# Kernel tuning notes

Hardware: AMD Instinct MI355X
Metric: run time of the kernel (lower is better)

The kernel has to match this reference:

```python
import jax, jax.numpy as jnp
import numpy as np
from math import sqrt

HEADS = 16
DIM_HEAD = 64
BETA = 1.0 / sqrt(DIM_HEAD)


def setup_inputs() -> dict:
    key = jax.random.key(0)
    k1, k2, k3 = jax.random.split(key, 3)
    b, n, dim = 2, 2048, 1024
    inner = HEADS * DIM_HEAD  # 1024
    x = jax.random.normal(k1, (b, n, dim), dtype=jnp.float32)
    W_qk = jax.random.normal(k2, (dim, 2 * inner), dtype=jnp.float32) * 0.02
    W_out = jax.random.normal(k3, (inner, dim), dtype=jnp.float32) * 0.02
    return {"x": x, "W_qk": W_qk, "W_out": W_out}


def reference(x, W_qk, W_out):
    # x: [b, n, dim]; to_qk: Linear(dim, 2*inner, bias=False)
    b, n, _ = x.shape
    qk = x @ W_qk                                   # [b, n, 2*inner]
    q, k = jnp.split(qk, 2, axis=-1)                # each [b, n, inner]
    # b n (h d) -> b h n d
    q = q.reshape(b, n, HEADS, DIM_HEAD).transpose(0, 2, 1, 3)
    k = k.reshape(b, n, HEADS, DIM_HEAD).transpose(0, 2, 1, 3)
    # beta-scaled scores
    scores = jnp.einsum('bhid,bhjd->bhij', q * BETA, k)  # [b, h, n, n]
    mask_value = -jnp.finfo(scores.dtype).max
    causal_mask = jnp.triu(jnp.ones((n, n), dtype=bool), k=1)
    scores = jnp.where(causal_mask, mask_value, scores)
    attn = jax.nn.softmax(scores, axis=-1)
    # K is reused as V
    out = jnp.einsum('bhij,bhjd->bhid', attn, k)    # [b, h, n, d]
    out = out.transpose(0, 2, 1, 3).reshape(b, n, HEADS * DIM_HEAD)
    # to_out Linear (dropout is identity in eval)
    return out @ W_out
```

## Files before the change

### kernel.cpp

```cpp
#include <hip/hip_runtime.h>
#include <hip/hip_bf16.h>
#include <math.h>

typedef short bf16x8 __attribute__((ext_vector_type(8)));
typedef float f32x4 __attribute__((ext_vector_type(4)));

__device__ __forceinline__ float bf2f(unsigned short u) {
    return __uint_as_float(((unsigned int)u) << 16);
}
__device__ __forceinline__ unsigned short f2bf(float f) {
    unsigned int u = __float_as_uint(f);
    u = (u + 0x7FFFu + ((u >> 16) & 1u)) >> 16;
    return (unsigned short)u;
}
__device__ __forceinline__ unsigned int pk2bf(float a, float b) {
    __hip_bfloat162 u = __float22bfloat162_rn(make_float2(a, b));
    return *(unsigned int*)&u;
}

#define ASYNC16(gp, lp)                                                        \
    __builtin_amdgcn_global_load_lds(                                          \
        (const __attribute__((address_space(1))) unsigned int*)(gp),           \
        (__attribute__((address_space(3))) unsigned int*)(lp), 16, 0, 0)

__global__ __launch_bounds__(256) void wtrans_kernel(const float* __restrict__ Wqk,
                                                     const float* __restrict__ Wout,
                                                     unsigned short* __restrict__ Wqk_t,
                                                     unsigned short* __restrict__ Wout_t) {
    const int z = blockIdx.z;
    const int N = z ? 1024 : 2048;
    if (z && blockIdx.y >= 32) return;
    const float* in = z ? Wout : Wqk;
    unsigned short* out = z ? Wout_t : Wqk_t;
    const int K = 1024;
    __shared__ float tile[32][33];
    int k0 = blockIdx.x * 32, n0 = blockIdx.y * 32;
    int tx = threadIdx.x & 31, ty = threadIdx.x >> 5;
    #pragma unroll
    for (int i = ty; i < 32; i += 8)
        tile[i][tx] = in[(size_t)(k0 + i) * N + (n0 + tx)];
    __syncthreads();
    #pragma unroll
    for (int i = ty; i < 32; i += 8)
        out[(size_t)(n0 + i) * K + (k0 + tx)] = f2bf(tile[tx][i]);
}

template <bool STORE_BF16, bool A_FP32, bool WRITE_KT>
__global__ __launch_bounds__(256) void gemm64_kernel(const void* __restrict__ Av,
                                                     const unsigned short* __restrict__ Bt,
                                                     void* __restrict__ C,
                                                     unsigned short* __restrict__ kT,
                                                     int K, int lda, int ldb, int ldc) {
    __shared__ unsigned short As[64 * 40];
    __shared__ unsigned short Bs[64 * 40];
    const int tid  = threadIdx.x;
    const int wave = tid >> 6;
    const int lane = tid & 63;
    const int quad = lane >> 4;
    const int lrow = lane & 15;
    const int m0 = blockIdx.x * 64;
    const int n0 = blockIdx.y * 64;
    const int ar = tid >> 2;
    const int ac = (tid & 3) * 8;

    f32x4 acc[4];
    #pragma unroll
    for (int t = 0; t < 4; ++t) { acc[t][0] = 0.f; acc[t][1] = 0.f; acc[t][2] = 0.f; acc[t][3] = 0.f; }

    const unsigned short* Bp = Bt + (size_t)(n0 + ar) * ldb + ac;

    for (int k0 = 0; k0 < K; k0 += 32) {
        bf16x8 bv = *(const bf16x8*)(Bp + k0);
        if (A_FP32) {
            const float* gx = (const float*)Av + (size_t)(m0 + ar) * lda + k0 + ac;
            float4 f0 = *(const float4*)(gx);
            float4 f1 = *(const float4*)(gx + 4);
            uint4 w = make_uint4(pk2bf(f0.x, f0.y), pk2bf(f0.z, f0.w),
                                 pk2bf(f1.x, f1.y), pk2bf(f1.z, f1.w));
            __syncthreads();
            *(uint4*)&As[ar * 40 + ac] = w;
        } else {
            bf16x8 av = *(const bf16x8*)((const unsigned short*)Av + (size_t)(m0 + ar) * lda + k0 + ac);
            __syncthreads();
            *(bf16x8*)&As[ar * 40 + ac] = av;
        }
        *(bf16x8*)&Bs[ar * 40 + ac] = bv;
        __syncthreads();
        bf16x8 afrag = *(const bf16x8*)&As[(wave * 16 + lrow) * 40 + quad * 8];
        #pragma unroll
        for (int t = 0; t < 4; ++t) {
            bf16x8 bfrag = *(const bf16x8*)&Bs[(t * 16 + lrow) * 40 + quad * 8];
            acc[t] = __builtin_amdgcn_mfma_f32_16x16x32_bf16(afrag, bfrag, acc[t], 0, 0, 0);
        }
    }

    const int row0 = m0 + wave * 16 + quad * 4;
    #pragma unroll
    for (int t = 0; t < 4; ++t) {
        const int cc = n0 + t * 16 + lrow;
        #pragma unroll
        for (int r = 0; r < 4; ++r) {
            if (STORE_BF16)
                ((unsigned short*)C)[(size_t)(row0 + r) * ldc + cc] = f2bf(acc[t][r]);
            else
                ((float*)C)[(size_t)(row0 + r) * ldc + cc] = acc[t][r];
        }
        if (WRITE_KT && cc >= 1024) {
            const int bb = row0 >> 11, tok = row0 & 2047;
            ushort4 v;
            v.x = f2bf(acc[t][0]); v.y = f2bf(acc[t][1]);
            v.z = f2bf(acc[t][2]); v.w = f2bf(acc[t][3]);
            *(ushort4*)(kT + ((size_t)(bb * 1024 + cc - 1024)) * 2048 + tok) = v;
        }
    }
}

#define LDK 72

__global__ __launch_bounds__(256) void attn_v5_kernel(const unsigned short* __restrict__ qkb,
                                                      const unsigned short* __restrict__ kT,
                                                      unsigned short* __restrict__ aout) {
    __shared__ unsigned short Kbuf[2][2][64 * 64];
    __shared__ unsigned short Ps[4][16 * LDK];

    const int bh = blockIdx.x;
    const int b = bh >> 4, h = bh & 15;
    const int qtile = 31 - (int)blockIdx.y;
    const int tid = threadIdx.x;
    const int wave = tid >> 6, lane = tid & 63, quad = lane >> 4, col = lane & 15;

    bf16x8 qa0, qa1;
    {
        const unsigned short* qp =
            qkb + ((size_t)(b * 2048 + qtile * 64 + wave * 16 + col)) * 2048 + h * 64;
        bf16x8 r0 = *(const bf16x8*)(qp + quad * 8);
        bf16x8 r1 = *(const bf16x8*)(qp + 32 + quad * 8);
        const float sc = 0.125f * 1.44269504088896f;
        #pragma unroll
        for (int i = 0; i < 8; ++i) {
            qa0[i] = (short)f2bf(bf2f((unsigned short)r0[i]) * sc);
            qa1[i] = (short)f2bf(bf2f((unsigned short)r1[i]) * sc);
        }
    }

    f32x4 accO[4];
    #pragma unroll
    for (int t = 0; t < 4; ++t) { accO[t][0] = 0.f; accO[t][1] = 0.f; accO[t][2] = 0.f; accO[t][3] = 0.f; }
    float lsum = 0.f;

    const int r8 = lane >> 3;
    const int c8 = (lane & 7) ^ r8;
    const unsigned short* knp =
        qkb + ((size_t)(b * 2048 + wave * 16 + r8)) * 2048 + 1024 + h * 64 + c8 * 8;
    const unsigned short* ktp = kT + ((size_t)(bh * 64 + wave * 16 + r8)) * 2048 + c8 * 8;

    auto issue = [&](int jt, int p) {
        const unsigned short* kn = knp + (size_t)jt * 64 * 2048;
        const unsigned short* kt = ktp + jt * 64;
        unsigned short* knl = &Kbuf[p][0][(wave * 16) * 64];
        unsigned short* ktl = &Kbuf[p][1][(wave * 16) * 64];
        ASYNC16(kn,            knl);
        ASYNC16(kn + 8 * 2048, knl + 8 * 64);
        ASYNC16(kt,            ktl);
        ASYNC16(kt + 8 * 2048, ktl + 8 * 64);
    };

    issue(0, 0);

    for (int jt = 0; jt <= qtile; ++jt) {
        const int cur = jt & 1;
        __builtin_amdgcn_s_barrier();
        if (jt < qtile) issue(jt + 1, cur ^ 1);
        if (jt < qtile) __builtin_amdgcn_s_waitcnt(0xF74);
        else            __builtin_amdgcn_s_waitcnt(0xF70);
        __builtin_amdgcn_s_barrier();
        __asm__ volatile("" ::: "memory");

        const unsigned short* Knc = &Kbuf[cur][0][0];
        const unsigned short* Ktc = &Kbuf[cur][1][0];

        const bool diag = (jt == qtile);
        const int tmax = diag ? wave : 3;

        float ls = 0.f;
        unsigned int pw[4][2];
        #pragma unroll
        for (int t = 0; t < 4; ++t) {
            if (t <= tmax) {
                const int row = (t * 16 + col) * 64;
                const int sw = col & 7;
                bf16x8 ka0 = *(const bf16x8*)&Knc[row + (quad ^ sw) * 8];
                bf16x8 ka1 = *(const bf16x8*)&Knc[row + ((4 + quad) ^ sw) * 8];
                f32x4 c = {-16.f, -16.f, -16.f, -16.f};
                c = __builtin_amdgcn_mfma_f32_16x16x32_bf16(ka0, qa0, c, 0, 0, 0);
                c = __builtin_amdgcn_mfma_f32_16x16x32_bf16(ka1, qa1, c, 0, 0, 0);
                if (diag && t == wave) {
                    #pragma unroll
                    for (int r = 0; r < 4; ++r)
                        if (quad * 4 + r > col) c[r] = -1e30f;
                }
                const float p0 = exp2f(c[0]);
                const float p1 = exp2f(c[1]);
                const float p2 = exp2f(c[2]);
                const float p3 = exp2f(c[3]);
                ls += (p0 + p1) + (p2 + p3);
                pw[t][0] = pk2bf(p0, p1);
                pw[t][1] = pk2bf(p2, p3);
            } else {
                pw[t][0] = 0u; pw[t][1] = 0u;
            }
        }
        lsum += ls;

        unsigned short* psb = &Ps[wave][col * LDK];
        #pragma unroll
        for (int t = 0; t < 4; ++t)
            *(uint2*)(psb + t * 16 + quad * 4) = make_uint2(pw[t][0], pw[t][1]);

        bf16x8 pa0 = *(const bf16x8*)(psb + quad * 8);
        bf16x8 pa1 = *(const bf16x8*)(psb + 32 + quad * 8);
        const bool hi = !(diag && wave < 2);

        #pragma unroll
        for (int t = 0; t < 4; ++t) {
            const int row = (t * 16 + col) * 64;
            const int sw = col & 7;
            bf16x8 vb0 = *(const bf16x8*)&Ktc[row + (quad ^ sw) * 8];
            accO[t] = __builtin_amdgcn_mfma_f32_16x16x32_bf16(pa0, vb0, accO[t], 0, 0, 0);
            if (hi) {
                bf16x8 vb1 = *(const bf16x8*)&Ktc[row + ((4 + quad) ^ sw) * 8];
                accO[t] = __builtin_amdgcn_mfma_f32_16x16x32_bf16(pa1, vb1, accO[t], 0, 0, 0);
            }
        }
    }

    lsum += __shfl_xor(lsum, 16);
    lsum += __shfl_xor(lsum, 32);
    #pragma unroll
    for (int r = 0; r < 4; ++r) {
        const float lr = __shfl(lsum, (lane & 48) | (quad * 4 + r));
        const float inv = 1.f / lr;
        const size_t row = (size_t)b * 2048 + qtile * 64 + wave * 16 + quad * 4 + r;
        unsigned short* op = aout + row * 1024 + h * 64;
        op[col]      = f2bf(accO[0][r] * inv);
        op[16 + col] = f2bf(accO[1][r] * inv);
        op[32 + col] = f2bf(accO[2][r] * inv);
        op[48 + col] = f2bf(accO[3][r] * inv);
    }
}

extern "C" void kernel_launch(void* const* d_in, const int* in_sizes, int n_in,
                              void* d_out, int out_size, void* d_ws, size_t ws_size,
                              hipStream_t stream) {
    (void)in_sizes; (void)n_in; (void)out_size; (void)ws_size;
    const float* x    = (const float*)d_in[0];
    const float* Wqk  = (const float*)d_in[1];
    const float* Wout = (const float*)d_in[2];
    float* out = (float*)d_out;

    unsigned short* kT     = (unsigned short*)d_ws;
    unsigned short* Wqk_t  = kT     + (size_t)2048 * 2048;
    unsigned short* Wout_t = Wqk_t  + (size_t)2048 * 1024;
    unsigned short* qkb    = Wout_t + (size_t)1024 * 1024;
    unsigned short* aoutb  = qkb    + (size_t)4096 * 2048;

    wtrans_kernel<<<dim3(32, 64, 2), dim3(256), 0, stream>>>(Wqk, Wout, Wqk_t, Wout_t);

    gemm64_kernel<true, true, true><<<dim3(64, 32), dim3(256), 0, stream>>>(
        (const void*)x, Wqk_t, (void*)qkb, kT, 1024, 1024, 1024, 2048);

    attn_v5_kernel<<<dim3(32, 32), dim3(256), 0, stream>>>(qkb, kT, aoutb);

    gemm64_kernel<false, false, false><<<dim3(64, 16), dim3(256), 0, stream>>>(
        (const void*)aoutb, Wout_t, (void*)out, nullptr, 1024, 1024, 1024, 1024);
}
```

Baseline: 197.1 us.

## Split x cast and K transpose out of GEMM, widen GEMM K-step to 64

Pre-casts x to bf16 in a separate kernel so the QK projection GEMM reads bf16 directly, and moves the strided K-transpose store out of the GEMM epilogue into a dedicated LDS-tiled transpose kernel. The GEMM main loop now stages 64-wide K slices per barrier pair, which halves the number of synchronisations. In exchange there are two extra launches and an extra round trip through global memory for x and K, and the kT buffer now aliases the xb workspace.

```diff
diff --git a/kernel.cpp b/kernel.cpp
--- a/kernel.cpp
+++ b/kernel.cpp
@@ -22,6 +22,18 @@
     __builtin_amdgcn_global_load_lds(                                          \
         (const __attribute__((address_space(1))) unsigned int*)(gp),           \
         (__attribute__((address_space(3))) unsigned int*)(lp), 16, 0, 0)
+
+__global__ __launch_bounds__(256) void cast_x_kernel(const float* __restrict__ in,
+                                                     unsigned short* __restrict__ out, int n) {
+    int i = (blockIdx.x * 256 + threadIdx.x) * 8;
+    if (i >= n) return;
+    float4 a = *(const float4*)(in + i);
+    float4 b = *(const float4*)(in + i + 4);
+    bf16x8 v;
+    v[0] = (short)f2bf(a.x); v[1] = (short)f2bf(a.y); v[2] = (short)f2bf(a.z); v[3] = (short)f2bf(a.w);
+    v[4] = (short)f2bf(b.x); v[5] = (short)f2bf(b.y); v[6] = (short)f2bf(b.z); v[7] = (short)f2bf(b.w);
+    *(bf16x8*)(out + i) = v;
+}
 
 __global__ __launch_bounds__(256) void wtrans_kernel(const float* __restrict__ Wqk,
                                                      const float* __restrict__ Wout,
@@ -45,14 +57,37 @@
         out[(size_t)(n0 + i) * K + (k0 + tx)] = f2bf(tile[tx][i]);
 }
 
-template <bool STORE_BF16, bool A_FP32, bool WRITE_KT>
-__global__ __launch_bounds__(256) void gemm64_kernel(const void* __restrict__ Av,
+__global__ __launch_bounds__(256) void ktrans_kernel(const unsigned short* __restrict__ qkb,
+                                                     unsigned short* __restrict__ kT) {
+    __shared__ unsigned short tl[64][68];
+    const int b = blockIdx.z;
+    const int tok0 = blockIdx.x * 64;
+    const int f0 = blockIdx.y * 64;
+    const int r = threadIdx.x >> 4;
+    const int c = (threadIdx.x & 15) * 4;
+    #pragma unroll
+    for (int i = 0; i < 4; ++i) {
+        const int rr = r + 16 * i;
+        ushort4 v = *(const ushort4*)(qkb + ((size_t)(b * 2048 + tok0 + rr)) * 2048 + 1024 + f0 + c);
+        *(ushort4*)&tl[rr][c] = v;
+    }
+    __syncthreads();
+    #pragma unroll
+    for (int i = 0; i < 4; ++i) {
+        const int fr = r + 16 * i;
+        ushort4 v;
+        v.x = tl[c + 0][fr]; v.y = tl[c + 1][fr]; v.z = tl[c + 2][fr]; v.w = tl[c + 3][fr];
+        *(ushort4*)(kT + ((size_t)(b * 1024 + f0 + fr)) * 2048 + tok0 + c) = v;
+    }
+}
+
+template <bool STORE_BF16>
+__global__ __launch_bounds__(256) void gemm64_kernel(const unsigned short* __restrict__ A,
                                                      const unsigned short* __restrict__ Bt,
                                                      void* __restrict__ C,
-                                                     unsigned short* __restrict__ kT,
                                                      int K, int lda, int ldb, int ldc) {
-    __shared__ unsigned short As[64 * 40];
-    __shared__ unsigned short Bs[64 * 40];
+    __shared__ unsigned short As[64 * 72];
+    __shared__ unsigned short Bs[64 * 72];
     const int tid  = threadIdx.x;
     const int wave = tid >> 6;
     const int lane = tid & 63;
@@ -67,30 +102,28 @@
     #pragma unroll
     for (int t = 0; t < 4; ++t) { acc[t][0] = 0.f; acc[t][1] = 0.f; acc[t][2] = 0.f; acc[t][3] = 0.f; }
 
+    const unsigned short* Ap = A  + (size_t)(m0 + ar) * lda + ac;
     const unsigned short* Bp = Bt + (size_t)(n0 + ar) * ldb + ac;
 
-    for (int k0 = 0; k0 < K; k0 += 32) {
-        bf16x8 bv = *(const bf16x8*)(Bp + k0);
-        if (A_FP32) {
-            const float* gx = (const float*)Av + (size_t)(m0 + ar) * lda + k0 + ac;
-            float4 f0 = *(const float4*)(gx);
-            float4 f1 = *(const float4*)(gx + 4);
-            uint4 w = make_uint4(pk2bf(f0.x, f0.y), pk2bf(f0.z, f0.w),
-                                 pk2bf(f1.x, f1.y), pk2bf(f1.z, f1.w));
-            __syncthreads();
-            *(uint4*)&As[ar * 40 + ac] = w;
-        } else {
-            bf16x8 av = *(const bf16x8*)((const unsigned short*)Av + (size_t)(m0 + ar) * lda + k0 + ac);
-            __syncthreads();
-            *(bf16x8*)&As[ar * 40 + ac] = av;
-        }
-        *(bf16x8*)&Bs[ar * 40 + ac] = bv;
+    for (int k0 = 0; k0 < K; k0 += 64) {
+        bf16x8 a0 = *(const bf16x8*)(Ap + k0);
+        bf16x8 a1 = *(const bf16x8*)(Ap + k0 + 32);
+        bf16x8 b0 = *(const bf16x8*)(Bp + k0);
+        bf16x8 b1 = *(const bf16x8*)(Bp + k0 + 32);
         __syncthreads();
-        bf16x8 afrag = *(const bf16x8*)&As[(wave * 16 + lrow) * 40 + quad * 8];
-        #pragma unroll
-        for (int t = 0; t < 4; ++t) {
-            bf16x8 bfrag = *(const bf16x8*)&Bs[(t * 16 + lrow) * 40 + quad * 8];
-            acc[t] = __builtin_amdgcn_mfma_f32_16x16x32_bf16(afrag, bfrag, acc[t], 0, 0, 0);
+        *(bf16x8*)&As[ar * 72 + ac]      = a0;
+        *(bf16x8*)&As[ar * 72 + 32 + ac] = a1;
+        *(bf16x8*)&Bs[ar * 72 + ac]      = b0;
+        *(bf16x8*)&Bs[ar * 72 + 32 + ac] = b1;
+        __syncthreads();
+        #pragma unroll
+        for (int h = 0; h < 2; ++h) {
+            bf16x8 afrag = *(const bf16x8*)&As[(wave * 16 + lrow) * 72 + h * 32 + quad * 8];
+            #pragma unroll
+            for (int t = 0; t < 4; ++t) {
+                bf16x8 bfrag = *(const bf16x8*)&Bs[(t * 16 + lrow) * 72 + h * 32 + quad * 8];
+                acc[t] = __builtin_amdgcn_mfma_f32_16x16x32_bf16(afrag, bfrag, acc[t], 0, 0, 0);
+            }
         }
     }
 
@@ -104,13 +137,6 @@
                 ((unsigned short*)C)[(size_t)(row0 + r) * ldc + cc] = f2bf(acc[t][r]);
             else
                 ((float*)C)[(size_t)(row0 + r) * ldc + cc] = acc[t][r];
-        }
-        if (WRITE_KT && cc >= 1024) {
-            const int bb = row0 >> 11, tok = row0 & 2047;
-            ushort4 v;
-            v.x = f2bf(acc[t][0]); v.y = f2bf(acc[t][1]);
-            v.z = f2bf(acc[t][2]); v.w = f2bf(acc[t][3]);
-            *(ushort4*)(kT + ((size_t)(bb * 1024 + cc - 1024)) * 2048 + tok) = v;
         }
     }
 }
@@ -258,19 +284,23 @@
     const float* Wout = (const float*)d_in[2];
     float* out = (float*)d_out;
 
-    unsigned short* kT     = (unsigned short*)d_ws;
-    unsigned short* Wqk_t  = kT     + (size_t)2048 * 2048;
+    unsigned short* xb     = (unsigned short*)d_ws;
+    unsigned short* Wqk_t  = xb     + (size_t)4096 * 1024;
     unsigned short* Wout_t = Wqk_t  + (size_t)2048 * 1024;
     unsigned short* qkb    = Wout_t + (size_t)1024 * 1024;
     unsigned short* aoutb  = qkb    + (size_t)4096 * 2048;
-
+    unsigned short* kT     = xb;
+
+    cast_x_kernel<<<dim3(2048), dim3(256), 0, stream>>>(x, xb, 4096 * 1024);
     wtrans_kernel<<<dim3(32, 64, 2), dim3(256), 0, stream>>>(Wqk, Wout, Wqk_t, Wout_t);
 
-    gemm64_kernel<true, true, true><<<dim3(64, 32), dim3(256), 0, stream>>>(
-        (const void*)x, Wqk_t, (void*)qkb, kT, 1024, 1024, 1024, 2048);
+    gemm64_kernel<true><<<dim3(64, 32), dim3(256), 0, stream>>>(
+        xb, Wqk_t, (void*)qkb, 1024, 1024, 1024, 2048);
+
+    ktrans_kernel<<<dim3(32, 16, 2), dim3(256), 0, stream>>>(qkb, kT);
 
     attn_v5_kernel<<<dim3(32, 32), dim3(256), 0, stream>>>(qkb, kT, aoutb);
 
-    gemm64_kernel<false, false, false><<<dim3(64, 16), dim3(256), 0, stream>>>(
-        (const void*)aoutb, Wout_t, (void*)out, nullptr, 1024, 1024, 1024, 1024);
-}
+    gemm64_kernel<false><<<dim3(64, 16), dim3(256), 0, stream>>>(
+        aoutb, Wout_t, (void*)out, 1024, 1024, 1024, 1024);
+}
```

New measurement: 199.2 us. Within noise of the previous version (+1.1%).
